# Performance work log

Hardware: AMD Instinct MI355X
Metric: run time of the kernel (lower is better)

Reference implementation:

```python
import jax, jax.numpy as jnp
import numpy as np

N_HEAD = 16
ROPE_BASE = 10000.0


def _rope_cos_sin(T, D, dtype):
    # inv_freq over even dims, freqs concatenated twice (rotate_half convention)
    inv_freq = 1.0 / (ROPE_BASE ** (jnp.arange(0, D, 2, dtype=jnp.float32) / D))
    t = jnp.arange(T, dtype=jnp.float32)
    freqs = jnp.outer(t, inv_freq)          # [T, D/2]
    emb = jnp.concatenate([freqs, freqs], axis=-1)  # [T, D]
    return jnp.cos(emb).astype(dtype), jnp.sin(emb).astype(dtype)


def _rotate_half(x):
    x1, x2 = jnp.split(x, 2, axis=-1)
    return jnp.concatenate([-x2, x1], axis=-1)


def setup_inputs() -> dict:
    key = jax.random.key(0)
    ks = jax.random.split(key, 5)
    B, T, C = 2, 2048, 1024
    s = 1.0 / np.sqrt(C)
    return {
        "x": jax.random.normal(ks[0], (B, T, C), jnp.float32),
        "W_attn": jax.random.normal(ks[1], (C, 3 * C), jnp.float32) * s,
        "b_attn": jax.random.normal(ks[2], (3 * C,), jnp.float32) * 0.02,
        "W_proj": jax.random.normal(ks[3], (C, C), jnp.float32) * s,
        "b_proj": jax.random.normal(ks[4], (C,), jnp.float32) * 0.02,
    }


def reference(x, W_attn, b_attn, W_proj, b_proj):
    B, T, C = x.shape
    H = N_HEAD
    D = C // H

    # fused QKV projection
    qkv = x @ W_attn + b_attn                      # [B, T, 3C]
    q, k, v = jnp.split(qkv, 3, axis=-1)
    q = q.reshape(B, T, H, D).transpose(0, 2, 1, 3)  # [B, H, T, D]
    k = k.reshape(B, T, H, D).transpose(0, 2, 1, 3)
    v = v.reshape(B, T, H, D).transpose(0, 2, 1, 3)

    # RoPE (no past_kv: applied to full q and k)
    cos, sin = _rope_cos_sin(T, D, x.dtype)        # [T, D]
    cos = cos[None, None]                          # [1, 1, T, D]
    sin = sin[None, None]
    q = q * cos + _rotate_half(q) * sin
    k = k * cos + _rotate_half(k) * sin

    # causal SDPA (dropout_p = 0 in reference)
    scale = 1.0 / np.sqrt(D)
    scores = jnp.einsum("bhqd,bhkd->bhqk", q, k) * scale
    causal = jnp.tril(jnp.ones((T, T), dtype=bool))
    scores = jnp.where(causal, scores, jnp.finfo(scores.dtype).min)
    attn = jax.nn.softmax(scores, axis=-1)
    y = jnp.einsum("bhqk,bhkd->bhqd", attn, v)     # [B, H, T, D]

    y = y.transpose(0, 2, 1, 3).reshape(B, T, C)
    y = y @ W_proj + b_proj
    return y
```

## Files before the change

### kernel.cpp

```cpp
#include <hip/hip_runtime.h>
#include <cstdint>
#include <cstddef>

#define SEQ_T 2048
#define NHEAD 16

typedef __attribute__((ext_vector_type(8))) short short8;
typedef __attribute__((ext_vector_type(4))) float f32x4;
typedef __attribute__((ext_vector_type(16))) float f32x16;

__device__ __forceinline__ unsigned short f2bf(float f) {
  union { float f; unsigned int u; } v; v.f = f;
  return (unsigned short)((v.u + 0x7FFFu + ((v.u >> 16) & 1u)) >> 16);
}
__device__ __forceinline__ float bf2f(unsigned short u) {
  union { unsigned int u; float f; } v; v.u = ((unsigned int)u) << 16;
  return v.f;
}

__device__ __forceinline__ unsigned cvtpk(float lo, float hi) {
  unsigned r;
  asm("v_cvt_pk_bf16_f32 %0, %1, %2" : "=v"(r) : "v"(lo), "v"(hi));
  return r;
}

__device__ __forceinline__ float max3f(float a, float b, float c) {
  float r;
  asm("v_max3_f32 %0, %1, %2, %3" : "=v"(r) : "v"(a), "v"(b), "v"(c));
  return r;
}

#if __has_builtin(__builtin_amdgcn_permlane32_swap)
__device__ __forceinline__ void plswap(unsigned& a, unsigned& b) {
  auto r = __builtin_amdgcn_permlane32_swap(a, b, false, false);
  a = r[0];
  b = r[1];
}
#else
__device__ __forceinline__ void plswap(unsigned& a, unsigned& b) {
  asm volatile("s_nop 1\n\tv_permlane32_swap_b32 %0, %1\n\ts_nop 1"
               : "+v"(a), "+v"(b));
}
#endif

__device__ __forceinline__ float xhalf_max(float x) {
  unsigned a = __builtin_bit_cast(unsigned, x), b = a;
  plswap(a, b);
  return fmaxf(__builtin_bit_cast(float, a), __builtin_bit_cast(float, b));
}
__device__ __forceinline__ float xhalf_add(float x) {
  unsigned a = __builtin_bit_cast(unsigned, x), b = a;
  plswap(a, b);
  return __builtin_bit_cast(float, a) + __builtin_bit_cast(float, b);
}

__device__ __forceinline__ float vmax16(const f32x16 v) {
  float m0 = max3f(v[0], v[1], v[2]);
  float m1 = max3f(v[3], v[4], v[5]);
  float m2 = max3f(v[6], v[7], v[8]);
  float m3 = max3f(v[9], v[10], v[11]);
  float m4 = max3f(v[12], v[13], v[14]);
  float m5 = max3f(m0, m1, v[15]);
  float m6 = max3f(m2, m3, m4);
  return fmaxf(m5, m6);
}

__device__ __forceinline__ void gl_lds16(const void* g, void* l) {
  __builtin_amdgcn_global_load_lds(
      (__attribute__((address_space(1))) void*)(void*)g,
      (__attribute__((address_space(3))) void*)l, 16, 0, 0);
}

__global__ void k_prep(const float* __restrict__ x,
                       const float* __restrict__ Wa,
                       const float* __restrict__ Wp,
                       unsigned short* __restrict__ xb,
                       unsigned short* __restrict__ wat,
                       unsigned short* __restrict__ wpt,
                       float2* __restrict__ tab) {
  const int b = blockIdx.x, tid = threadIdx.x;
  if (b < 4096) {
    int i = b * 256 + tid;
    float4 v = ((const float4*)x)[i];
    unsigned long long pk = (unsigned long long)f2bf(v.x)
                          | ((unsigned long long)f2bf(v.y) << 16)
                          | ((unsigned long long)f2bf(v.z) << 32)
                          | ((unsigned long long)f2bf(v.w) << 48);
    ((unsigned long long*)xb)[i] = pk;
  } else if (b < 5632) {
    int idx = (b - 4096) * 256 + tid;
    int n = idx % 3072, k0 = (idx / 3072) * 8;
    short8 v;
#pragma unroll
    for (int j = 0; j < 8; ++j)
      v[j] = (short)f2bf(Wa[(size_t)(k0 + j) * 3072 + n]);
    *(short8*)&wat[(size_t)n * 1024 + k0] = v;
  } else if (b < 6144) {
    int idx = (b - 5632) * 256 + tid;
    int n = idx & 1023, k0 = (idx >> 10) * 8;
    short8 v;
#pragma unroll
    for (int j = 0; j < 8; ++j)
      v[j] = (short)f2bf(Wp[(size_t)(k0 + j) * 1024 + n]);
    *(short8*)&wpt[(size_t)n * 1024 + k0] = v;
  } else {
    int idx = (b - 6144) * 256 + tid;
    int t = idx >> 5, i = idx & 31;
    float inv = powf(10000.0f, -(float)(2 * i) / 64.0f);
    float f = (float)t * inv;
    tab[idx] = make_float2(cosf(f), sinf(f));
  }
}

__global__ void k_gemm_qkv(const unsigned short* __restrict__ A,
                           const unsigned short* __restrict__ Bt,
                           const float* __restrict__ bias,
                           const float2* __restrict__ cs,
                           unsigned short* __restrict__ qo,
                           unsigned short* __restrict__ ko,
                           unsigned short* __restrict__ vo) {
  __shared__ unsigned short lA[128 * 32];
  __shared__ unsigned short lB[128 * 32];
  const int K = 1024;
  const int bn = blockIdx.x, bm = blockIdx.y;
  const int tid = threadIdx.x, w = tid >> 6, l = tid & 63;
  const int lr = l & 15, lh = l >> 4;
  const int wm = w >> 1, wn = w & 1;

  f32x4 acc[4][4];
#pragma unroll
  for (int m = 0; m < 4; ++m)
#pragma unroll
    for (int n = 0; n < 4; ++n)
#pragma unroll
      for (int i = 0; i < 4; ++i) acc[m][n][i] = 0.f;

  const unsigned short* ga0 = A + (size_t)(bm * 128 + w * 16 + (l >> 2)) * K + (l & 3) * 8;
  const unsigned short* gb0 = Bt + (size_t)(bn * 128 + w * 16 + (l >> 2)) * K + (l & 3) * 8;
  unsigned short* la0 = &lA[w * 512];
  unsigned short* la1 = &lA[(w + 4) * 512];
  unsigned short* lb0 = &lB[w * 512];
  unsigned short* lb1 = &lB[(w + 4) * 512];

  for (int kt = 0; kt < K; kt += 32) {
    gl_lds16(ga0 + kt, la0);
    gl_lds16(ga0 + (size_t)64 * K + kt, la1);
    gl_lds16(gb0 + kt, lb0);
    gl_lds16(gb0 + (size_t)64 * K + kt, lb1);
    __syncthreads();
    short8 af[4], bf[4];
#pragma unroll
    for (int m = 0; m < 4; ++m) af[m] = *(const short8*)&lA[(wm * 64 + m * 16 + lr) * 32 + lh * 8];
#pragma unroll
    for (int n = 0; n < 4; ++n) bf[n] = *(const short8*)&lB[(wn * 64 + n * 16 + lr) * 32 + lh * 8];
#pragma unroll
    for (int m = 0; m < 4; ++m)
#pragma unroll
      for (int n = 0; n < 4; ++n)
        acc[m][n] = __builtin_amdgcn_mfma_f32_16x16x32_bf16(af[m], bf[n], acc[m][n], 0, 0, 0);
    __syncthreads();
  }

  const int col0 = bn * 128 + wn * 64;
  const int row0 = bm * 128 + wm * 64;
  const int sec = col0 >> 10;
  const int hh = (col0 >> 6) & 15;
  float bl[4];
#pragma unroll
  for (int n = 0; n < 4; ++n) bl[n] = bias[col0 + n * 16 + lr];

  if (sec == 2) {
    const int b = row0 >> 11;
    unsigned short* vtp = vo + (size_t)(b * 16 + hh) * 64 * 2048;
#pragma unroll
    for (int n = 0; n < 4; ++n) {
      int d = n * 16 + lr;
#pragma unroll
      for (int m = 0; m < 4; ++m) {
        int t = (row0 + m * 16 + lh * 4) & 2047;
        unsigned long long pk = (unsigned long long)f2bf(acc[m][n][0] + bl[n])
                              | ((unsigned long long)f2bf(acc[m][n][1] + bl[n]) << 16)
                              | ((unsigned long long)f2bf(acc[m][n][2] + bl[n]) << 32)
                              | ((unsigned long long)f2bf(acc[m][n][3] + bl[n]) << 48);
        *(unsigned long long*)&vtp[(size_t)d * 2048 + t] = pk;
      }
    }
  } else {
    unsigned short* dst = (sec == 0) ? qo : ko;
#pragma unroll
    for (int m = 0; m < 4; ++m)
#pragma unroll
      for (int i = 0; i < 4; ++i) {
        int row = row0 + m * 16 + lh * 4 + i;
        int t = row & 2047, b = row >> 11;
        size_t ob = ((size_t)(b * 16 + hh) * 2048 + t) * 64;
#pragma unroll
        for (int n = 0; n < 4; ++n) {
          float v = acc[m][n][i] + bl[n];
          float pv = acc[m][n ^ 2][i] + bl[n ^ 2];
          int d = n * 16 + lr;
          float2 c = cs[t * 32 + (d & 31)];
          float rot = (d < 32) ? -pv : pv;
          dst[ob + d] = f2bf(v * c.x + rot * c.y);
        }
      }
  }
}

__global__ __launch_bounds__(512, 4) void k_attn(const unsigned short* __restrict__ Q,
                       const unsigned short* __restrict__ Kg,
                       const unsigned short* __restrict__ VT,
                       unsigned short* __restrict__ P0,
                       unsigned short* __restrict__ P1,
                       float2* __restrict__ ML) {
  __shared__ unsigned short smem[16896];
  const int id = blockIdx.x;
  const int xcd = id & 7, u = id >> 3;
  const int a = u & 31, sweep = u >> 5;
  const int g = a & 3, j = a >> 2;
  const int bh = xcd * 4 + g;
  const int qt = (sweep & 1) ? (15 - j) : j;
  const int sp = sweep >> 1;
  const int tid = threadIdx.x, w = tid >> 6, l = tid & 63;
  const int wq = w & 3, wk = w >> 2;
  const int lq = l & 31, hi = l >> 5;
  const size_t base = (size_t)bh * SEQ_T * 64;
  const float CE = 0.18033688f;
  const float DTHR = 44.3614f;

  const int qrow = qt * 128 + wq * 32 + lq;
  short8 qf[4];
#pragma unroll
  for (int c = 0; c < 4; ++c)
    qf[c] = *(const short8*)&Q[base + (size_t)qrow * 64 + c * 16 + hi * 8];

  const int r0 = tid >> 3, c8 = tid & 7;
  const unsigned short* ks0 = Kg + base + (size_t)r0 * 64 + ((c8 ^ (r0 & 7)) * 8);
  const unsigned short* vs0 = VT + base + (size_t)r0 * 2048 + ((c8 ^ (r0 & 7)) * 8);

#define STAGE(KT, B) do { \
    gl_lds16(ks0 + (size_t)(KT) * 4096, &smem[(B) * 4096 + w * 512]); \
    gl_lds16(vs0 + (size_t)(KT) * 64,   &smem[8192 + (B) * 4096 + w * 512]); \
  } while (0)

  float mi = -1.0e30f, li = 0.f;
  f32x16 oc0, oc1;
#pragma unroll
  for (int r = 0; r < 16; ++r) { oc0[r] = 0.f; oc1[r] = 0.f; }

  const int nit = qt + 1;
  const int kt0 = sp * nit;
  const int mfrom = 2 * qt;
  STAGE(kt0, 0);
  __syncthreads();

  for (int it = 0; it < nit; ++it) {
    const int cur = it & 1;
    const int kt = kt0 + it;
    if (it + 1 < nit) STAGE(kt + 1, cur ^ 1);
    const unsigned short* kb = &smem[cur * 4096];
    const unsigned short* vb = &smem[8192 + cur * 4096];

    f32x16 st;
#pragma unroll
    for (int r = 0; r < 16; ++r) st[r] = 0.f;
    __builtin_amdgcn_s_setprio(1);
#pragma unroll
    for (int c = 0; c < 4; ++c) {
      const short8 kf = *(const short8*)&kb[(wk * 32 + lq) * 64 + (((2 * c + hi) ^ (lq & 7)) * 8)];
      st = __builtin_amdgcn_mfma_f32_32x32x16_bf16(kf, qf[c], st, 0, 0, 0);
    }
    __builtin_amdgcn_s_setprio(0);

    if (kt >= mfrom) {
#pragma unroll
      for (int r = 0; r < 16; ++r) {
        int kvg = kt * 64 + wk * 32 + (r & 3) + 8 * (r >> 2) + 4 * hi;
        if (kvg > qrow) st[r] = -3.0e38f;
      }
    }

    float tm = xhalf_max(vmax16(st));
    if (!__all(tm <= mi + DTHR)) {
      float mn = fmaxf(mi, tm);
      float scq = exp2f((mi - mn) * CE);
      mi = mn;
      li *= scq;
#pragma unroll
      for (int r = 0; r < 16; ++r) {
        float sc_r = __shfl(scq, (r & 3) + 8 * (r >> 2) + 4 * hi, 64);
        oc0[r] *= sc_r;
        oc1[r] *= sc_r;
      }
    }
    const float nb = mi * CE;
    float rs = 0.f;
#pragma unroll
    for (int r = 0; r < 16; ++r) {
      float p = exp2f(fmaf(st[r], CE, -nb));
      st[r] = p;
      rs += p;
    }
    li += rs;

    short8 pa[2];
#pragma unroll
    for (int kc = 0; kc < 2; ++kc) {
      const int o = kc * 8;
      unsigned w0 = cvtpk(st[o + 0], st[o + 1]);
      unsigned w1 = cvtpk(st[o + 2], st[o + 3]);
      unsigned w2 = cvtpk(st[o + 4], st[o + 5]);
      unsigned w3 = cvtpk(st[o + 6], st[o + 7]);
      plswap(w0, w2);
      plswap(w1, w3);
      uint4 F;
      F.x = w0; F.y = w1; F.z = w2; F.w = w3;
      pa[kc] = __builtin_bit_cast(short8, F);
    }

    {
      short8 vbf[2][2];
#pragma unroll
      for (int dt = 0; dt < 2; ++dt)
#pragma unroll
        for (int kc = 0; kc < 2; ++kc)
          vbf[dt][kc] = *(const short8*)&vb[(dt * 32 + lq) * 64 +
                          (((wk * 4 + kc * 2 + hi) ^ (lq & 7)) * 8)];
      __builtin_amdgcn_s_setprio(1);
#pragma unroll
      for (int kc = 0; kc < 2; ++kc) {
        oc0 = __builtin_amdgcn_mfma_f32_32x32x16_bf16(pa[kc], vbf[0][kc], oc0, 0, 0, 0);
        oc1 = __builtin_amdgcn_mfma_f32_32x32x16_bf16(pa[kc], vbf[1][kc], oc1, 0, 0, 0);
      }
      __builtin_amdgcn_s_setprio(0);
    }

    if (it + 1 < nit) __syncthreads();
  }

  li = xhalf_add(li);

  __syncthreads();
  float* obuf = (float*)smem;
  float* mlb  = (float*)&smem[16384];
  if (wk == 1) {
#pragma unroll
    for (int r = 0; r < 16; ++r) {
      const int q = (r & 3) + 8 * (r >> 2) + 4 * hi;
      obuf[wq * 2048 + q * 64 + lq]      = oc0[r];
      obuf[wq * 2048 + q * 64 + 32 + lq] = oc1[r];
    }
    if (hi == 0) {
      mlb[wq * 64 + lq * 2 + 0] = mi;
      mlb[wq * 64 + lq * 2 + 1] = li;
    }
  }
  __syncthreads();
  if (wk == 0) {
    unsigned short* dst = sp ? P1 : P0;
    const int hh = bh & 15, bb = bh >> 4;
#pragma unroll
    for (int r = 0; r < 16; ++r) {
      const int q = (r & 3) + 8 * (r >> 2) + 4 * hi;
      float m0 = __shfl(mi, q, 64), l0 = __shfl(li, q, 64);
      float m1 = mlb[wq * 64 + q * 2 + 0], l1 = mlb[wq * 64 + q * 2 + 1];
      float mm = fmaxf(m0, m1);
      float f0 = exp2f((m0 - mm) * CE), f1 = exp2f((m1 - mm) * CE);
      float dn = f0 * l0 + f1 * l1;
      float inv = (dn > 0.f) ? (1.0f / dn) : 0.f;
      float o0 = (f0 * oc0[r] + f1 * obuf[wq * 2048 + q * 64 + lq]) * inv;
      float o1 = (f0 * oc1[r] + f1 * obuf[wq * 2048 + q * 64 + 32 + lq]) * inv;
      int qg = qt * 128 + wq * 32 + q;
      size_t ob = (size_t)(bb * 2048 + qg) * 1024 + hh * 64;
      dst[ob + lq]      = f2bf(o0);
      dst[ob + 32 + lq] = f2bf(o1);
      if (lq == 0) ML[(size_t)(sp * 32 + bh) * 2048 + qg] = make_float2(mm, dn);
    }
  }
#undef STAGE
}

__global__ void k_combine(const unsigned short* __restrict__ P1,
                          const float2* __restrict__ ML,
                          unsigned short* __restrict__ P0) {
  const float CE = 0.18033688f;
  int idx = blockIdx.x * 256 + threadIdx.x;
  int flat = idx * 8;
  int c = flat & 1023, t = (flat >> 10) & 2047, b = flat >> 21;
  int bh = b * 16 + (c >> 6);
  float2 a0 = ML[(size_t)bh * 2048 + t];
  float2 a1 = ML[(size_t)(32 + bh) * 2048 + t];
  float mm = fmaxf(a0.x, a1.x);
  float w0 = exp2f((a0.x - mm) * CE) * a0.y;
  float w1 = exp2f((a1.x - mm) * CE) * a1.y;
  float inv = 1.0f / (w0 + w1);
  w0 *= inv; w1 *= inv;
  short8 o0 = *(const short8*)&P0[flat];
  short8 o1 = *(const short8*)&P1[flat];
  short8 o;
#pragma unroll
  for (int k = 0; k < 8; ++k)
    o[k] = (short)f2bf(w0 * bf2f((unsigned short)o0[k]) + w1 * bf2f((unsigned short)o1[k]));
  *(short8*)&P0[flat] = o;
}

__global__ void k_gemm_proj(const unsigned short* __restrict__ A,
                            const unsigned short* __restrict__ Bt,
                            const float* __restrict__ bias,
                            float* __restrict__ out) {
  __shared__ unsigned short lA[64 * 32];
  __shared__ unsigned short lB[128 * 32];
  const int K = 1024;
  const int bn = blockIdx.x, bm = blockIdx.y;
  const int tid = threadIdx.x, w = tid >> 6, l = tid & 63;
  const int lr = l & 15, lh = l >> 4;
  const int wm = w >> 1, wn = w & 1;

  f32x4 acc[2][4];
#pragma unroll
  for (int m = 0; m < 2; ++m)
#pragma unroll
    for (int n = 0; n < 4; ++n)
#pragma unroll
      for (int i = 0; i < 4; ++i) acc[m][n][i] = 0.f;

  const unsigned short* ga0 = A + (size_t)(bm * 64 + (tid >> 2)) * K + (tid & 3) * 8;
  const unsigned short* gb0 = Bt + (size_t)(bn * 128 + w * 16 + (l >> 2)) * K + (l & 3) * 8;
  unsigned short* la0 = &lA[w * 512];
  unsigned short* lb0 = &lB[w * 512];
  unsigned short* lb1 = &lB[(w + 4) * 512];

  for (int kt = 0; kt < K; kt += 32) {
    gl_lds16(ga0 + kt, la0);
    gl_lds16(gb0 + kt, lb0);
    gl_lds16(gb0 + (size_t)64 * K + kt, lb1);
    __syncthreads();
    short8 af[2], bf[4];
#pragma unroll
    for (int m = 0; m < 2; ++m) af[m] = *(const short8*)&lA[(wm * 32 + m * 16 + lr) * 32 + lh * 8];
#pragma unroll
    for (int n = 0; n < 4; ++n) bf[n] = *(const short8*)&lB[(wn * 64 + n * 16 + lr) * 32 + lh * 8];
#pragma unroll
    for (int m = 0; m < 2; ++m)
#pragma unroll
      for (int n = 0; n < 4; ++n)
        acc[m][n] = __builtin_amdgcn_mfma_f32_16x16x32_bf16(af[m], bf[n], acc[m][n], 0, 0, 0);
    __syncthreads();
  }

  const int col0 = bn * 128 + wn * 64;
  const int row0 = bm * 64 + wm * 32;
  float bl[4];
#pragma unroll
  for (int n = 0; n < 4; ++n) bl[n] = bias[col0 + n * 16 + lr];
#pragma unroll
  for (int m = 0; m < 2; ++m)
#pragma unroll
    for (int i = 0; i < 4; ++i) {
      int row = row0 + m * 16 + lh * 4 + i;
#pragma unroll
      for (int n = 0; n < 4; ++n)
        out[(size_t)row * 1024 + col0 + n * 16 + lr] = acc[m][n][i] + bl[n];
    }
}

extern "C" void kernel_launch(void* const* d_in, const int* in_sizes, int n_in,
                              void* d_out, int out_size, void* d_ws, size_t ws_size,
                              hipStream_t stream) {
  const float* x     = (const float*)d_in[0];
  const float* Wattn = (const float*)d_in[1];
  const float* battn = (const float*)d_in[2];
  const float* Wproj = (const float*)d_in[3];
  const float* bproj = (const float*)d_in[4];
  float* out = (float*)d_out;

  char* ws = (char*)d_ws;
  unsigned short* xb  = (unsigned short*)(ws);
  unsigned short* wat = (unsigned short*)(ws + (8ull  << 20));
  unsigned short* wpt = (unsigned short*)(ws + (14ull << 20));
  unsigned short* qa  = (unsigned short*)(ws + (16ull << 20));
  unsigned short* ka  = (unsigned short*)(ws + (24ull << 20));
  unsigned short* va  = (unsigned short*)(ws + (32ull << 20));
  unsigned short* ob  = (unsigned short*)(ws + (40ull << 20));
  float2* cs          = (float2*)(ws + (48ull << 20));
  float2* ml          = (float2*)wat;

  k_prep<<<6400, 256, 0, stream>>>(x, Wattn, Wproj, xb, wat, wpt, cs);
  k_gemm_qkv<<<dim3(24, 32), 256, 0, stream>>>(xb, wat, battn, cs, qa, ka, va);
  k_attn<<<1024, 512, 0, stream>>>(qa, ka, va, ob, xb, ml);
  k_combine<<<2048, 256, 0, stream>>>(xb, ml, ob);
  k_gemm_proj<<<dim3(8, 64), 256, 0, stream>>>(ob, wpt, bproj, out);
}
```

Before: 124.0 us.

## Split long causal query tiles four ways in attention and remap GEMM block order

Attention key-range splitting now gives the later half of query tiles (qt>=8) four splits instead of two, which evens out per-block work and adds blocks. Two extra partial-output buffers hold these splits, and the combine kernel merges four partials for the latter half of rows. The mode is chosen from the workspace size, with a fallback to the old scheme. Both GEMMs switch to a 1D grid with an XCD-aware block-index remap meant to improve L2 reuse. In exchange, combine reads more data and the ML table grows into the reused weight buffer.

```diff
diff --git a/kernel.cpp b/kernel.cpp
--- a/kernel.cpp
+++ b/kernel.cpp
@@ -122,7 +122,10 @@
   __shared__ unsigned short lA[128 * 32];
   __shared__ unsigned short lB[128 * 32];
   const int K = 1024;
-  const int bn = blockIdx.x, bm = blockIdx.y;
+  const int id_ = blockIdx.x;
+  const int u_ = id_ >> 3;
+  const int bn = (id_ & 7) * 3 + u_ % 3;
+  const int bm = u_ / 3;
   const int tid = threadIdx.x, w = tid >> 6, l = tid & 63;
   const int lr = l & 15, lh = l >> 4;
   const int wm = w >> 1, wn = w & 1;
@@ -212,15 +215,28 @@
                        const unsigned short* __restrict__ VT,
                        unsigned short* __restrict__ P0,
                        unsigned short* __restrict__ P1,
-                       float2* __restrict__ ML) {
+                       unsigned short* __restrict__ P2,
+                       unsigned short* __restrict__ P3,
+                       float2* __restrict__ ML,
+                       int mode) {
   __shared__ unsigned short smem[16896];
   const int id = blockIdx.x;
   const int xcd = id & 7, u = id >> 3;
-  const int a = u & 31, sweep = u >> 5;
-  const int g = a & 3, j = a >> 2;
+  int g, qt, sp;
+  if (mode) {
+    g = u & 3;
+    const int v = u >> 2;
+    if (v < 32) { qt = 15 - (v >> 2); sp = v & 3; }
+    else        { const int v2 = v - 32; qt = 7 - (v2 >> 1); sp = v2 & 1; }
+  } else {
+    const int a = u & 31, sweep = u >> 5;
+    g = a & 3;
+    const int j = a >> 2;
+    qt = (sweep & 1) ? (15 - j) : j;
+    sp = sweep >> 1;
+  }
+  const int sh = (mode && qt >= 8) ? 2 : 1;
   const int bh = xcd * 4 + g;
-  const int qt = (sweep & 1) ? (15 - j) : j;
-  const int sp = sweep >> 1;
   const int tid = threadIdx.x, w = tid >> 6, l = tid & 63;
   const int wq = w & 3, wk = w >> 2;
   const int lq = l & 31, hi = l >> 5;
@@ -248,8 +264,9 @@
 #pragma unroll
   for (int r = 0; r < 16; ++r) { oc0[r] = 0.f; oc1[r] = 0.f; }
 
-  const int nit = qt + 1;
-  const int kt0 = sp * nit;
+  const int tot = 2 * (qt + 1);
+  const int kt0 = (sp * tot) >> sh;
+  const int nit = (((sp + 1) * tot) >> sh) - kt0;
   const int mfrom = 2 * qt;
   STAGE(kt0, 0);
   __syncthreads();
@@ -357,8 +374,8 @@
   }
   __syncthreads();
   if (wk == 0) {
-    unsigned short* dst = sp ? P1 : P0;
     const int hh = bh & 15, bb = bh >> 4;
+    unsigned short* dst = (sp == 0) ? P0 : (sp == 1) ? P1 : (sp == 2) ? P2 : P3;
 #pragma unroll
     for (int r = 0; r < 16; ++r) {
       const int q = (r & 3) + 8 * (r >> 2) + 4 * hi;
@@ -371,18 +388,23 @@
       float o0 = (f0 * oc0[r] + f1 * obuf[wq * 2048 + q * 64 + lq]) * inv;
       float o1 = (f0 * oc1[r] + f1 * obuf[wq * 2048 + q * 64 + 32 + lq]) * inv;
       int qg = qt * 128 + wq * 32 + q;
-      size_t ob = (size_t)(bb * 2048 + qg) * 1024 + hh * 64;
+      size_t ob = (sp < 2)
+          ? ((size_t)(bb * 2048 + qg) * 1024 + hh * 64)
+          : ((size_t)(bb * 1024 + (qg - 1024)) * 1024 + hh * 64);
       dst[ob + lq]      = f2bf(o0);
       dst[ob + 32 + lq] = f2bf(o1);
-      if (lq == 0) ML[(size_t)(sp * 32 + bh) * 2048 + qg] = make_float2(mm, dn);
+      if (lq == 0) ML[((size_t)sp * 32 + bh) * 2048 + qg] = make_float2(mm, dn);
     }
   }
 #undef STAGE
 }
 
 __global__ void k_combine(const unsigned short* __restrict__ P1,
+                          const unsigned short* __restrict__ P2,
+                          const unsigned short* __restrict__ P3,
                           const float2* __restrict__ ML,
-                          unsigned short* __restrict__ P0) {
+                          unsigned short* __restrict__ P0,
+                          int mode) {
   const float CE = 0.18033688f;
   int idx = blockIdx.x * 256 + threadIdx.x;
   int flat = idx * 8;
@@ -390,17 +412,36 @@
   int bh = b * 16 + (c >> 6);
   float2 a0 = ML[(size_t)bh * 2048 + t];
   float2 a1 = ML[(size_t)(32 + bh) * 2048 + t];
-  float mm = fmaxf(a0.x, a1.x);
-  float w0 = exp2f((a0.x - mm) * CE) * a0.y;
-  float w1 = exp2f((a1.x - mm) * CE) * a1.y;
-  float inv = 1.0f / (w0 + w1);
-  w0 *= inv; w1 *= inv;
   short8 o0 = *(const short8*)&P0[flat];
   short8 o1 = *(const short8*)&P1[flat];
   short8 o;
-#pragma unroll
-  for (int k = 0; k < 8; ++k)
-    o[k] = (short)f2bf(w0 * bf2f((unsigned short)o0[k]) + w1 * bf2f((unsigned short)o1[k]));
+  if (mode && t >= 1024) {
+    float2 a2 = ML[(size_t)(64 + bh) * 2048 + t];
+    float2 a3 = ML[(size_t)(96 + bh) * 2048 + t];
+    size_t f2 = ((size_t)(b * 1024 + (t - 1024)) * 1024) + c;
+    short8 o2 = *(const short8*)&P2[f2];
+    short8 o3 = *(const short8*)&P3[f2];
+    float mm = fmaxf(fmaxf(a0.x, a1.x), fmaxf(a2.x, a3.x));
+    float w0 = exp2f((a0.x - mm) * CE) * a0.y;
+    float w1 = exp2f((a1.x - mm) * CE) * a1.y;
+    float w2 = exp2f((a2.x - mm) * CE) * a2.y;
+    float w3 = exp2f((a3.x - mm) * CE) * a3.y;
+    float inv = 1.0f / (w0 + w1 + w2 + w3);
+    w0 *= inv; w1 *= inv; w2 *= inv; w3 *= inv;
+#pragma unroll
+    for (int k = 0; k < 8; ++k)
+      o[k] = (short)f2bf(w0 * bf2f((unsigned short)o0[k]) + w1 * bf2f((unsigned short)o1[k])
+                       + w2 * bf2f((unsigned short)o2[k]) + w3 * bf2f((unsigned short)o3[k]));
+  } else {
+    float mm = fmaxf(a0.x, a1.x);
+    float w0 = exp2f((a0.x - mm) * CE) * a0.y;
+    float w1 = exp2f((a1.x - mm) * CE) * a1.y;
+    float inv = 1.0f / (w0 + w1);
+    w0 *= inv; w1 *= inv;
+#pragma unroll
+    for (int k = 0; k < 8; ++k)
+      o[k] = (short)f2bf(w0 * bf2f((unsigned short)o0[k]) + w1 * bf2f((unsigned short)o1[k]));
+  }
   *(short8*)&P0[flat] = o;
 }
 
@@ -411,7 +452,8 @@
   __shared__ unsigned short lA[64 * 32];
   __shared__ unsigned short lB[128 * 32];
   const int K = 1024;
-  const int bn = blockIdx.x, bm = blockIdx.y;
+  const int bn = blockIdx.x & 7;
+  const int bm = blockIdx.x >> 3;
   const int tid = threadIdx.x, w = tid >> 6, l = tid & 63;
   const int lr = l & 15, lh = l >> 4;
   const int wm = w >> 1, wn = w & 1;
@@ -485,9 +527,14 @@
   float2* cs          = (float2*)(ws + (48ull << 20));
   float2* ml          = (float2*)wat;
 
+  const bool big = ws_size >= (57ull << 20);
+  unsigned short* p2 = big ? (unsigned short*)(ws + (48ull << 20) + (512ull << 10)) : ob;
+  unsigned short* p3 = big ? (unsigned short*)(ws + (52ull << 20) + (512ull << 10)) : ob;
+  const int mode = big ? 1 : 0;
+
   k_prep<<<6400, 256, 0, stream>>>(x, Wattn, Wproj, xb, wat, wpt, cs);
-  k_gemm_qkv<<<dim3(24, 32), 256, 0, stream>>>(xb, wat, battn, cs, qa, ka, va);
-  k_attn<<<1024, 512, 0, stream>>>(qa, ka, va, ob, xb, ml);
-  k_combine<<<2048, 256, 0, stream>>>(xb, ml, ob);
-  k_gemm_proj<<<dim3(8, 64), 256, 0, stream>>>(ob, wpt, bproj, out);
-}
+  k_gemm_qkv<<<768, 256, 0, stream>>>(xb, wat, battn, cs, qa, ka, va);
+  k_attn<<<mode ? 1536 : 1024, 512, 0, stream>>>(qa, ka, va, ob, xb, p2, p3, ml, mode);
+  k_combine<<<2048, 256, 0, stream>>>(xb, p2, p3, ml, ob, mode);
+  k_gemm_proj<<<512, 256, 0, stream>>>(ob, wpt, bproj, out);
+}
```

After: 128.3 us. 1.04x slower.

## Fuse split-K attention combine into projection GEMM A-tile load

Applied to the files above, without the earlier changes.

Removes the separate combine kernel and instead merges the two partial attention outputs using their max/denominator stats while loading A tiles in the projection GEMM. This saves a kernel launch and a full write plus re-read of the combined buffer. In exchange, the combine math is recomputed by each of the 8 N-column blocks, and the A load becomes a synchronous register load plus an LDS store instead of an async global-to-LDS copy.

```diff
diff --git a/kernel.cpp b/kernel.cpp
--- a/kernel.cpp
+++ b/kernel.cpp
@@ -380,31 +380,9 @@
 #undef STAGE
 }
 
-__global__ void k_combine(const unsigned short* __restrict__ P1,
-                          const float2* __restrict__ ML,
-                          unsigned short* __restrict__ P0) {
-  const float CE = 0.18033688f;
-  int idx = blockIdx.x * 256 + threadIdx.x;
-  int flat = idx * 8;
-  int c = flat & 1023, t = (flat >> 10) & 2047, b = flat >> 21;
-  int bh = b * 16 + (c >> 6);
-  float2 a0 = ML[(size_t)bh * 2048 + t];
-  float2 a1 = ML[(size_t)(32 + bh) * 2048 + t];
-  float mm = fmaxf(a0.x, a1.x);
-  float w0 = exp2f((a0.x - mm) * CE) * a0.y;
-  float w1 = exp2f((a1.x - mm) * CE) * a1.y;
-  float inv = 1.0f / (w0 + w1);
-  w0 *= inv; w1 *= inv;
-  short8 o0 = *(const short8*)&P0[flat];
-  short8 o1 = *(const short8*)&P1[flat];
-  short8 o;
-#pragma unroll
-  for (int k = 0; k < 8; ++k)
-    o[k] = (short)f2bf(w0 * bf2f((unsigned short)o0[k]) + w1 * bf2f((unsigned short)o1[k]));
-  *(short8*)&P0[flat] = o;
-}
-
-__global__ void k_gemm_proj(const unsigned short* __restrict__ A,
+__global__ void k_gemm_proj(const unsigned short* __restrict__ P0,
+                            const unsigned short* __restrict__ P1,
+                            const float2* __restrict__ ML,
                             const unsigned short* __restrict__ Bt,
                             const float* __restrict__ bias,
                             float* __restrict__ out) {
@@ -415,6 +393,7 @@
   const int tid = threadIdx.x, w = tid >> 6, l = tid & 63;
   const int lr = l & 15, lh = l >> 4;
   const int wm = w >> 1, wn = w & 1;
+  const float CE = 0.18033688f;
 
   f32x4 acc[2][4];
 #pragma unroll
@@ -424,16 +403,36 @@
 #pragma unroll
       for (int i = 0; i < 4; ++i) acc[m][n][i] = 0.f;
 
-  const unsigned short* ga0 = A + (size_t)(bm * 64 + (tid >> 2)) * K + (tid & 3) * 8;
+  const int arow = bm * 64 + (tid >> 2);
+  const int t_ = arow & 2047, b_ = arow >> 11;
+  const size_t aoff = (size_t)arow * 1024 + (tid & 3) * 8;
+  unsigned short* lwa = &lA[(tid >> 2) * 32 + (tid & 3) * 8];
+  const float2* ml0 = ML + (size_t)(b_ * 16) * 2048 + t_;
+
   const unsigned short* gb0 = Bt + (size_t)(bn * 128 + w * 16 + (l >> 2)) * K + (l & 3) * 8;
-  unsigned short* la0 = &lA[w * 512];
   unsigned short* lb0 = &lB[w * 512];
   unsigned short* lb1 = &lB[(w + 4) * 512];
 
   for (int kt = 0; kt < K; kt += 32) {
-    gl_lds16(ga0 + kt, la0);
     gl_lds16(gb0 + kt, lb0);
     gl_lds16(gb0 + (size_t)64 * K + kt, lb1);
+    {
+      const int hh = kt >> 6;
+      float2 a0 = ml0[(size_t)hh * 2048];
+      float2 a1 = ml0[(size_t)(32 * 2048) + hh * 2048];
+      float mm = fmaxf(a0.x, a1.x);
+      float w0 = exp2f((a0.x - mm) * CE) * a0.y;
+      float w1 = exp2f((a1.x - mm) * CE) * a1.y;
+      float inv = 1.0f / (w0 + w1);
+      w0 *= inv; w1 *= inv;
+      short8 o0 = *(const short8*)&P0[aoff + kt];
+      short8 o1 = *(const short8*)&P1[aoff + kt];
+      short8 oa;
+#pragma unroll
+      for (int k = 0; k < 8; ++k)
+        oa[k] = (short)f2bf(w0 * bf2f((unsigned short)o0[k]) + w1 * bf2f((unsigned short)o1[k]));
+      *(short8*)lwa = oa;
+    }
     __syncthreads();
     short8 af[2], bf[4];
 #pragma unroll
@@ -488,6 +487,5 @@
   k_prep<<<6400, 256, 0, stream>>>(x, Wattn, Wproj, xb, wat, wpt, cs);
   k_gemm_qkv<<<dim3(24, 32), 256, 0, stream>>>(xb, wat, battn, cs, qa, ka, va);
   k_attn<<<1024, 512, 0, stream>>>(qa, ka, va, ob, xb, ml);
-  k_combine<<<2048, 256, 0, stream>>>(xb, ml, ob);
-  k_gemm_proj<<<dim3(8, 64), 256, 0, stream>>>(ob, wpt, bproj, out);
-}
+  k_gemm_proj<<<dim3(8, 64), 256, 0, stream>>>(ob, xb, ml, wpt, bproj, out);
+}
```

New measurement: 132.1 us. 1.07x slower.

## Triple-buffer K tiles with two-ahead prefetch and partial vmcnt waits in attention

Applied to the files above, without the earlier changes.

The attention kernel now keeps three K buffers in LDS and prefetches K two iterations ahead, while V stays double-buffered one iteration ahead. The full __syncthreads at the end of each iteration becomes an explicit s_waitcnt vmcnt(1) plus s_barrier, so the K load issued for the tile after next can stay in flight across the barrier. This is meant to hide global-to-LDS latency for K. In exchange LDS use per block grows, which could reduce occupancy, and correctness now relies on the manual wait counts matching the order the loads are issued.

```diff
diff --git a/kernel.cpp b/kernel.cpp
--- a/kernel.cpp
+++ b/kernel.cpp
@@ -213,7 +213,7 @@
                        unsigned short* __restrict__ P0,
                        unsigned short* __restrict__ P1,
                        float2* __restrict__ ML) {
-  __shared__ unsigned short smem[16896];
+  __shared__ unsigned short smem[20480];
   const int id = blockIdx.x;
   const int xcd = id & 7, u = id >> 3;
   const int a = u & 31, sweep = u >> 5;
@@ -238,11 +238,6 @@
   const unsigned short* ks0 = Kg + base + (size_t)r0 * 64 + ((c8 ^ (r0 & 7)) * 8);
   const unsigned short* vs0 = VT + base + (size_t)r0 * 2048 + ((c8 ^ (r0 & 7)) * 8);
 
-#define STAGE(KT, B) do { \
-    gl_lds16(ks0 + (size_t)(KT) * 4096, &smem[(B) * 4096 + w * 512]); \
-    gl_lds16(vs0 + (size_t)(KT) * 64,   &smem[8192 + (B) * 4096 + w * 512]); \
-  } while (0)
-
   float mi = -1.0e30f, li = 0.f;
   f32x16 oc0, oc1;
 #pragma unroll
@@ -251,15 +246,23 @@
   const int nit = qt + 1;
   const int kt0 = sp * nit;
   const int mfrom = 2 * qt;
-  STAGE(kt0, 0);
+
+  gl_lds16(ks0 + (size_t)kt0 * 4096, &smem[w * 512]);
+  if (nit > 1) gl_lds16(ks0 + (size_t)(kt0 + 1) * 4096, &smem[4096 + w * 512]);
+  gl_lds16(vs0 + (size_t)kt0 * 64, &smem[12288 + w * 512]);
   __syncthreads();
 
+  int kcur = 0;
   for (int it = 0; it < nit; ++it) {
-    const int cur = it & 1;
     const int kt = kt0 + it;
-    if (it + 1 < nit) STAGE(kt + 1, cur ^ 1);
-    const unsigned short* kb = &smem[cur * 4096];
-    const unsigned short* vb = &smem[8192 + cur * 4096];
+    if (it + 1 < nit)
+      gl_lds16(vs0 + (size_t)(kt + 1) * 64, &smem[12288 + (((it + 1) & 1)) * 4096 + w * 512]);
+    if (it + 2 < nit) {
+      const int kst = (kcur == 0) ? 2 : kcur - 1;
+      gl_lds16(ks0 + (size_t)(kt + 2) * 4096, &smem[kst * 4096 + w * 512]);
+    }
+    const unsigned short* kb = &smem[kcur * 4096];
+    const unsigned short* vb = &smem[12288 + (it & 1) * 4096];
 
     f32x16 st;
 #pragma unroll
@@ -335,7 +338,13 @@
       __builtin_amdgcn_s_setprio(0);
     }
 
-    if (it + 1 < nit) __syncthreads();
+    if (it + 1 < nit) {
+      if (it + 2 < nit) asm volatile("s_waitcnt vmcnt(1)" ::: "memory");
+      else              asm volatile("s_waitcnt vmcnt(0)" ::: "memory");
+      __builtin_amdgcn_s_barrier();
+      __builtin_amdgcn_sched_barrier(0);
+    }
+    kcur = (kcur == 2) ? 0 : kcur + 1;
   }
 
   li = xhalf_add(li);
@@ -377,7 +386,6 @@
       if (lq == 0) ML[(size_t)(sp * 32 + bh) * 2048 + qg] = make_float2(mm, dn);
     }
   }
-#undef STAGE
 }
 
 __global__ void k_combine(const unsigned short* __restrict__ P1,
```

Measured after the change: 124.9 us. About the same (+0.8%).
